# Kernel tuning notes

Hardware: AMD Instinct MI355X
Metric: run time of the kernel (lower is better)

## Reference

```python
import jax, jax.numpy as jnp
import numpy as np

G = 8
NEIGHBORS = 9
EPS = 1e-5


def grid_sample_bilinear_border(img, grid):
    # img: [B, C, H, W], grid: [B, Hg, Wg, 2] with (x, y) in [-1, 1]
    # matches torch.nn.functional.grid_sample(mode='bilinear', padding_mode='border', align_corners=False)
    B, C, H, W = img.shape
    gx, gy = grid[..., 0], grid[..., 1]
    ix = jnp.clip(((gx + 1.0) * W - 1.0) * 0.5, 0.0, W - 1.0)
    iy = jnp.clip(((gy + 1.0) * H - 1.0) * 0.5, 0.0, H - 1.0)
    x0 = jnp.floor(ix); y0 = jnp.floor(iy)
    x1 = x0 + 1.0;      y1 = y0 + 1.0
    w00 = (x1 - ix) * (y1 - iy)
    w01 = (ix - x0) * (y1 - iy)
    w10 = (x1 - ix) * (iy - y0)
    w11 = (ix - x0) * (iy - y0)
    x0i = jnp.clip(x0, 0, W - 1).astype(jnp.int32)
    x1i = jnp.clip(x1, 0, W - 1).astype(jnp.int32)
    y0i = jnp.clip(y0, 0, H - 1).astype(jnp.int32)
    y1i = jnp.clip(y1, 0, H - 1).astype(jnp.int32)

    def gather(im, yy, xx):  # im [C,H,W], yy/xx [Hg,Wg] -> [C,Hg,Wg]
        return im[:, yy, xx]

    g = jax.vmap(gather)
    out = (g(img, y0i, x0i) * w00[:, None]
         + g(img, y0i, x1i) * w01[:, None]
         + g(img, y1i, x0i) * w10[:, None]
         + g(img, y1i, x1i) * w11[:, None])
    return out  # [B, C, Hg, Wg]


def pconv(x, w):
    # 1x1x1 conv3d (no bias): x [B,Cin,D,H,W], w [Cout,Cin]
    return jnp.einsum('bcdhw,oc->bodhw', x, w)


def bn_relu(x, gamma, beta):
    # BatchNorm3d (training-mode batch stats, biased variance) + ReLU
    mean = jnp.mean(x, axis=(0, 2, 3, 4), keepdims=True)
    var = jnp.var(x, axis=(0, 2, 3, 4), keepdims=True)
    xn = (x - mean) * jax.lax.rsqrt(var + EPS)
    return jax.nn.relu(xn * gamma.reshape(1, -1, 1, 1, 1) + beta.reshape(1, -1, 1, 1, 1))


def setup_inputs() -> dict:
    key = jax.random.key(0)
    ks = jax.random.split(key, 8)
    B, C, H, W = 2, 64, 256, 320
    ref_feature = jax.random.normal(ks[0], (B, C, H, W), dtype=jnp.float32)
    grid = jax.random.uniform(ks[1], (B, NEIGHBORS * H, W, 2), dtype=jnp.float32,
                              minval=-1.0, maxval=1.0)
    s0 = 1.0 / np.sqrt(G)
    w0 = jax.random.uniform(ks[2], (16, G), jnp.float32, -s0, s0)
    g0 = jnp.ones((16,), jnp.float32); b0 = jnp.zeros((16,), jnp.float32)
    s1 = 1.0 / np.sqrt(16)
    w1 = jax.random.uniform(ks[3], (8, 16), jnp.float32, -s1, s1)
    g1 = jnp.ones((8,), jnp.float32); b1 = jnp.zeros((8,), jnp.float32)
    s2 = 1.0 / np.sqrt(8)
    ws = jax.random.uniform(ks[4], (1, 8), jnp.float32, -s2, s2)
    bs = jax.random.uniform(ks[5], (1,), jnp.float32, -s2, s2)
    return {"ref_feature": ref_feature, "grid": grid,
            "w0": w0, "g0": g0, "b0": b0,
            "w1": w1, "g1": g1, "b1": b1,
            "ws": ws, "bs": bs}


def reference(ref_feature, grid, w0, g0, b0, w1, g1, b1, ws, bs):
    B, C, H, W = ref_feature.shape
    x = grid_sample_bilinear_border(ref_feature, grid)          # [B, C, 9H, W]
    ref = ref_feature.reshape(B, G, C // G, H, W)               # [B, G, C/G, H, W]
    x = x.reshape(B, G, C // G, NEIGHBORS, H, W)
    x = jnp.mean(x * ref[:, :, :, None], axis=2)                # [B, G, 9, H, W]
    x = bn_relu(pconv(x, w0), g0, b0)                           # [B, 16, 9, H, W]
    x = bn_relu(pconv(x, w1), g1, b1)                           # [B, 8, 9, H, W]
    s = pconv(x, ws) + bs.reshape(1, -1, 1, 1, 1)               # [B, 1, 9, H, W]
    return jax.nn.sigmoid(jnp.squeeze(s, axis=1))               # [B, 9, H, W]
```

## Files before the change

### kernel.cpp

```cpp
#include <hip/hip_runtime.h>
#include <math.h>


constexpr int   Bc  = 2;
constexpr int   Cc  = 64;
constexpr int   Hc  = 256;
constexpr int   Wc  = 320;
constexpr int   NBc = 9;
constexpr int   HWc = Hc * Wc;
constexpr int   NPIX = Bc * HWc;
constexpr int   NPT  = Bc * NBc * HWc;
constexpr float EPSV = 1e-5f;

constexpr int NBLK_S = NPIX / 32;
constexpr int NBT4   = NPT / 1024;

constexpr size_t OFF_FEATB = 0;
constexpr size_t OFF_SB    = OFF_FEATB + (size_t)NPIX * 32;
constexpr size_t OFF_P1    = 0;
constexpr size_t OFF_P2    = OFF_P1 + (size_t)NBT4 * 64;
constexpr size_t OFF_PAR1  = OFF_P2 + (size_t)NBT4 * 16;
constexpr size_t OFF_PAR2  = OFF_PAR1 + 272;

__device__ __forceinline__ unsigned short f2bf_rne(float v) {
  unsigned int u = __float_as_uint(v);
  unsigned int r = (u + 0x7fffu + ((u >> 16) & 1u)) >> 16;
  return (unsigned short)r;
}
__device__ __forceinline__ void unpack8(uint4 u, float f[8]) {
  f[0] = __uint_as_float(u.x << 16);
  f[1] = __uint_as_float(u.x & 0xffff0000u);
  f[2] = __uint_as_float(u.y << 16);
  f[3] = __uint_as_float(u.y & 0xffff0000u);
  f[4] = __uint_as_float(u.z << 16);
  f[5] = __uint_as_float(u.z & 0xffff0000u);
  f[6] = __uint_as_float(u.w << 16);
  f[7] = __uint_as_float(u.w & 0xffff0000u);
}
__device__ __forceinline__ float dot8(const float s[8], float4 wa, float4 wb) {
  return s[0] * wa.x + s[1] * wa.y + s[2] * wa.z + s[3] * wa.w +
         s[4] * wb.x + s[5] * wb.y + s[6] * wb.z + s[7] * wb.w;
}

__global__ __launch_bounds__(256) void k_transpose(
    const float* __restrict__ feat, unsigned short* __restrict__ featB) {
  __shared__ float lds[64][65];
  const int tid  = threadIdx.x;
  const int b    = blockIdx.x / (HWc / 64);
  const int tile = blockIdx.x % (HWc / 64);
  const int hw0  = tile * 64;
  const int p    = tid & 63;
  const int ty   = tid >> 6;

  const float* src = feat + (size_t)b * Cc * HWc + hw0 + p;
#pragma unroll
  for (int c0 = 0; c0 < 64; c0 += 4) {
    lds[c0 + ty][p] = src[(size_t)(c0 + ty) * HWc];
  }
  __syncthreads();
  const int ch = tid & 63;
  unsigned short* dst = featB + ((size_t)b * HWc + hw0) * 64 + ch;
#pragma unroll
  for (int p0 = 0; p0 < 64; p0 += 4) {
    dst[(size_t)(p0 + ty) * 64] = f2bf_rne(lds[ch][p0 + ty]);
  }
}

__global__ __launch_bounds__(256) void k_sample(
    const float* __restrict__ grid, const unsigned short* __restrict__ featB,
    unsigned short* __restrict__ sOut) {
  const int tid = threadIdx.x;
  const int cid = blockIdx.x * 32 + (tid >> 3);
  const int j   = tid & 7;
  const int b   = cid / HWc;
  const int hw  = cid - b * HWc;
  const int h   = hw / Wc;
  const int w   = hw - h * Wc;

  const uint4* fbAll = (const uint4*)featB;
  const uint4 ur = fbAll[(size_t)cid * 8 + j];
  float r[8];
  unpack8(ur, r);

  const uint4* fb = fbAll + (size_t)b * HWc * 8;

#pragma unroll 3
  for (int n = 0; n < NBc; ++n) {
    const size_t gi = ((((size_t)b * NBc + n) * Hc + h) * Wc + w) * 2;
    const float2 g2 = *(const float2*)(grid + gi);
    float ix = ((g2.x + 1.f) * (float)Wc - 1.f) * 0.5f;
    float iy = ((g2.y + 1.f) * (float)Hc - 1.f) * 0.5f;
    ix = fminf(fmaxf(ix, 0.f), (float)(Wc - 1));
    iy = fminf(fmaxf(iy, 0.f), (float)(Hc - 1));
    const float x0f = floorf(ix), y0f = floorf(iy);
    const float fx = ix - x0f, fy = iy - y0f;
    const int x0 = (int)x0f, y0 = (int)y0f;
    const int x1 = min(x0 + 1, Wc - 1), y1 = min(y0 + 1, Hc - 1);
    const float w00 = (1.f - fx) * (1.f - fy);
    const float w01 = fx * (1.f - fy);
    const float w10 = (1.f - fx) * fy;
    const float w11 = fx * fy;

    const uint4 u00 = fb[(size_t)(y0 * Wc + x0) * 8 + j];
    const uint4 u01 = fb[(size_t)(y0 * Wc + x1) * 8 + j];
    const uint4 u10 = fb[(size_t)(y1 * Wc + x0) * 8 + j];
    const uint4 u11 = fb[(size_t)(y1 * Wc + x1) * 8 + j];
    float a[8], c[8], d[8], e[8];
    unpack8(u00, a);
    unpack8(u01, c);
    unpack8(u10, d);
    unpack8(u11, e);

    float s = 0.f;
#pragma unroll
    for (int k = 0; k < 8; ++k) {
      s += (w00 * a[k] + w01 * c[k] + w10 * d[k] + w11 * e[k]) * r[k];
    }
    s *= 0.125f;

    const size_t pt = ((size_t)b * NBc + n) * HWc + hw;
    sOut[pt * 8 + j] = f2bf_rne(s);
  }
}

__global__ __launch_bounds__(256) void k_stats1(
    const unsigned short* __restrict__ sB, float* __restrict__ part1) {
  const int tid = threadIdx.x;
  float acc[44];
#pragma unroll
  for (int i = 0; i < 44; ++i) acc[i] = 0.f;

  const uint4* src = (const uint4*)sB + (size_t)blockIdx.x * 1024 + tid;
#pragma unroll
  for (int i = 0; i < 4; ++i) {
    float s[8];
    unpack8(src[i * 256], s);
#pragma unroll
    for (int j = 0; j < 8; ++j) acc[j] += s[j];
#pragma unroll
    for (int j = 0; j < 8; ++j) {
#pragma unroll
      for (int k = 0; k <= j; ++k) {
        acc[8 + j * (j + 1) / 2 + k] += s[j] * s[k];
      }
    }
  }
  __shared__ float red[4 * 44];
  const int wid = tid >> 6;
#pragma unroll
  for (int i = 0; i < 44; ++i) {
    float v = acc[i];
#pragma unroll
    for (int off = 32; off; off >>= 1) v += __shfl_xor(v, off);
    if ((tid & 63) == 0) red[wid * 44 + i] = v;
  }
  __syncthreads();
  if (tid < 44) {
    part1[blockIdx.x * 64 + tid] =
        red[tid] + red[44 + tid] + red[88 + tid] + red[132 + tid];
  }
}

__global__ __launch_bounds__(256) void k_reduce1(
    const float* __restrict__ part1, const float* __restrict__ w0,
    const float* __restrict__ w1, const float* __restrict__ g0,
    const float* __restrict__ b0, float* __restrict__ par1) {
  __shared__ float red[1024], totm[64], a1s[16];
  const int tid = threadIdx.x;
  {
    const int cq = tid & 15, chk = tid >> 4;
    float4 a = make_float4(0.f, 0.f, 0.f, 0.f);
    for (int r = chk; r < NBT4; r += 16) {
      const float4 v = *(const float4*)(part1 + r * 64 + cq * 4);
      a.x += v.x; a.y += v.y; a.z += v.z; a.w += v.w;
    }
    red[chk * 64 + cq * 4 + 0] = a.x;
    red[chk * 64 + cq * 4 + 1] = a.y;
    red[chk * 64 + cq * 4 + 2] = a.z;
    red[chk * 64 + cq * 4 + 3] = a.w;
  }
  __syncthreads();
  if (tid < 64) {
    float v = 0.f;
#pragma unroll
    for (int k = 0; k < 16; ++k) v += red[k * 64 + tid];
    totm[tid] = v;
  }
  __syncthreads();
  if (tid < 16) {
    float wr[8];
    float mean = 0.f, ey2 = 0.f;
#pragma unroll
    for (int j = 0; j < 8; ++j) {
      wr[j] = w0[tid * 8 + j];
      mean += wr[j] * totm[j];
    }
#pragma unroll
    for (int j = 0; j < 8; ++j) {
#pragma unroll
      for (int k = 0; k <= j; ++k) {
        const float v = wr[j] * wr[k] * totm[8 + j * (j + 1) / 2 + k];
        ey2 += (k == j) ? v : 2.f * v;
      }
    }
    const float invN = 1.f / (float)NPT;
    mean *= invN;
    ey2 *= invN;
    const float var = ey2 - mean * mean;
    const float a = g0[tid] * rsqrtf(var + EPSV);
    a1s[tid] = a;
    par1[128 + tid] = b0[tid] - mean * a;
  }
  __syncthreads();
  if (tid < 128) {
    par1[tid] = a1s[tid >> 3] * w0[tid];
    par1[144 + (tid & 15) * 8 + (tid >> 4)] = w1[tid];
  }
}

__global__ __launch_bounds__(256) void k_stats2(
    const unsigned short* __restrict__ sB, const float* __restrict__ par1,
    float* __restrict__ part2) {
  __shared__ float w0ps[128], c1vs[16], w1ts[128];
  __shared__ float red[64];
  const int tid = threadIdx.x;
  if (tid < 128) {
    w0ps[tid] = par1[tid];
    w1ts[tid] = par1[144 + tid];
  }
  if (tid >= 128 && tid < 144) c1vs[tid - 128] = par1[tid];
  __syncthreads();

  const uint4* src = (const uint4*)sB + (size_t)blockIdx.x * 1024 + tid;
  float s0[8], s1[8], s2[8], s3[8];
  unpack8(src[0], s0);
  unpack8(src[256], s1);
  unpack8(src[512], s2);
  unpack8(src[768], s3);

  float z0[8], z1[8], z2[8], z3[8];
#pragma unroll
  for (int o = 0; o < 8; ++o) { z0[o] = 0.f; z1[o] = 0.f; z2[o] = 0.f; z3[o] = 0.f; }
#pragma unroll
  for (int c = 0; c < 16; ++c) {
    const float4 wa = *(const float4*)(w0ps + c * 8);
    const float4 wb = *(const float4*)(w0ps + c * 8 + 4);
    const float cc = c1vs[c];
    const float4 ta = *(const float4*)(w1ts + c * 8);
    const float4 tb = *(const float4*)(w1ts + c * 8 + 4);
    const float xa = fmaxf(dot8(s0, wa, wb) + cc, 0.f);
    const float xb = fmaxf(dot8(s1, wa, wb) + cc, 0.f);
    const float xc = fmaxf(dot8(s2, wa, wb) + cc, 0.f);
    const float xd = fmaxf(dot8(s3, wa, wb) + cc, 0.f);
    z0[0] += ta.x * xa; z0[1] += ta.y * xa; z0[2] += ta.z * xa; z0[3] += ta.w * xa;
    z0[4] += tb.x * xa; z0[5] += tb.y * xa; z0[6] += tb.z * xa; z0[7] += tb.w * xa;
    z1[0] += ta.x * xb; z1[1] += ta.y * xb; z1[2] += ta.z * xb; z1[3] += ta.w * xb;
    z1[4] += tb.x * xb; z1[5] += tb.y * xb; z1[6] += tb.z * xb; z1[7] += tb.w * xb;
    z2[0] += ta.x * xc; z2[1] += ta.y * xc; z2[2] += ta.z * xc; z2[3] += ta.w * xc;
    z2[4] += tb.x * xc; z2[5] += tb.y * xc; z2[6] += tb.z * xc; z2[7] += tb.w * xc;
    z3[0] += ta.x * xd; z3[1] += ta.y * xd; z3[2] += ta.z * xd; z3[3] += ta.w * xd;
    z3[4] += tb.x * xd; z3[5] += tb.y * xd; z3[6] += tb.z * xd; z3[7] += tb.w * xd;
  }

  const int wid = tid >> 6;
#pragma unroll
  for (int o = 0; o < 8; ++o) {
    float v = (z0[o] + z1[o]) + (z2[o] + z3[o]);
    float v2 = (z0[o] * z0[o] + z1[o] * z1[o]) + (z2[o] * z2[o] + z3[o] * z3[o]);
#pragma unroll
    for (int off = 32; off; off >>= 1) {
      v += __shfl_xor(v, off);
      v2 += __shfl_xor(v2, off);
    }
    if ((tid & 63) == 0) {
      red[wid * 16 + o] = v;
      red[wid * 16 + 8 + o] = v2;
    }
  }
  __syncthreads();
  if (tid < 16) {
    part2[blockIdx.x * 16 + tid] =
        red[tid] + red[16 + tid] + red[32 + tid] + red[48 + tid];
  }
}

__global__ __launch_bounds__(256) void k_reduce2(
    const float* __restrict__ part2, const float* __restrict__ g1,
    const float* __restrict__ b1, const float* __restrict__ wsW,
    const float* __restrict__ bs, float* __restrict__ par2) {
  __shared__ float red[1024], totz[16];
  const int tid = threadIdx.x;
  {
    const int cq = tid & 3, chk = tid >> 2;
    float4 a = make_float4(0.f, 0.f, 0.f, 0.f);
    for (int r = chk; r < NBT4; r += 64) {
      const float4 v = *(const float4*)(part2 + r * 16 + cq * 4);
      a.x += v.x; a.y += v.y; a.z += v.z; a.w += v.w;
    }
    red[chk * 16 + cq * 4 + 0] = a.x;
    red[chk * 16 + cq * 4 + 1] = a.y;
    red[chk * 16 + cq * 4 + 2] = a.z;
    red[chk * 16 + cq * 4 + 3] = a.w;
  }
  __syncthreads();
  if (tid < 16) {
    float v = 0.f;
#pragma unroll
    for (int k = 0; k < 64; ++k) v += red[k * 16 + tid];
    totz[tid] = v;
  }
  __syncthreads();
  if (tid < 8) {
    const float invN = 1.f / (float)NPT;
    const float mean = totz[tid] * invN;
    const float var = totz[8 + tid] * invN - mean * mean;
    const float a = g1[tid] * rsqrtf(var + EPSV);
    par2[tid * 4 + 0] = a;
    par2[tid * 4 + 1] = b1[tid] - mean * a;
    par2[tid * 4 + 2] = wsW[tid];
    par2[tid * 4 + 3] = 0.f;
  }
  if (tid == 8) par2[32] = bs[0];
}

__global__ __launch_bounds__(256) void k_final(
    const unsigned short* __restrict__ sB, const float* __restrict__ par1,
    const float* __restrict__ par2, float* __restrict__ out) {
  __shared__ float w0ps[128], c1vs[16], w1ts[128], w2s[33];
  const int tid = threadIdx.x;
  if (tid < 128) {
    w0ps[tid] = par1[tid];
    w1ts[tid] = par1[144 + tid];
  }
  if (tid >= 128 && tid < 144) c1vs[tid - 128] = par1[tid];
  if (tid >= 160 && tid < 193) w2s[tid - 160] = par2[tid - 160];
  __syncthreads();

  const uint4* src = (const uint4*)sB + (size_t)blockIdx.x * 1024 + tid;
  float s0[8], s1[8], s2[8], s3[8];
  unpack8(src[0], s0);
  unpack8(src[256], s1);
  unpack8(src[512], s2);
  unpack8(src[768], s3);

  float z0[8], z1[8], z2[8], z3[8];
#pragma unroll
  for (int o = 0; o < 8; ++o) { z0[o] = 0.f; z1[o] = 0.f; z2[o] = 0.f; z3[o] = 0.f; }
#pragma unroll
  for (int c = 0; c < 16; ++c) {
    const float4 wa = *(const float4*)(w0ps + c * 8);
    const float4 wb = *(const float4*)(w0ps + c * 8 + 4);
    const float cc = c1vs[c];
    const float4 ta = *(const float4*)(w1ts + c * 8);
    const float4 tb = *(const float4*)(w1ts + c * 8 + 4);
    const float xa = fmaxf(dot8(s0, wa, wb) + cc, 0.f);
    const float xb = fmaxf(dot8(s1, wa, wb) + cc, 0.f);
    const float xc = fmaxf(dot8(s2, wa, wb) + cc, 0.f);
    const float xd = fmaxf(dot8(s3, wa, wb) + cc, 0.f);
    z0[0] += ta.x * xa; z0[1] += ta.y * xa; z0[2] += ta.z * xa; z0[3] += ta.w * xa;
    z0[4] += tb.x * xa; z0[5] += tb.y * xa; z0[6] += tb.z * xa; z0[7] += tb.w * xa;
    z1[0] += ta.x * xb; z1[1] += ta.y * xb; z1[2] += ta.z * xb; z1[3] += ta.w * xb;
    z1[4] += tb.x * xb; z1[5] += tb.y * xb; z1[6] += tb.z * xb; z1[7] += tb.w * xb;
    z2[0] += ta.x * xc; z2[1] += ta.y * xc; z2[2] += ta.z * xc; z2[3] += ta.w * xc;
    z2[4] += tb.x * xc; z2[5] += tb.y * xc; z2[6] += tb.z * xc; z2[7] += tb.w * xc;
    z3[0] += ta.x * xd; z3[1] += ta.y * xd; z3[2] += ta.z * xd; z3[3] += ta.w * xd;
    z3[4] += tb.x * xd; z3[5] += tb.y * xd; z3[6] += tb.z * xd; z3[7] += tb.w * xd;
  }

  const float bsr = w2s[32];
  float r0 = bsr, r1 = bsr, r2 = bsr, r3 = bsr;
#pragma unroll
  for (int o = 0; o < 8; ++o) {
    const float4 pr = *(const float4*)(w2s + o * 4);
    r0 += pr.z * fmaxf(fmaf(pr.x, z0[o], pr.y), 0.f);
    r1 += pr.z * fmaxf(fmaf(pr.x, z1[o], pr.y), 0.f);
    r2 += pr.z * fmaxf(fmaf(pr.x, z2[o], pr.y), 0.f);
    r3 += pr.z * fmaxf(fmaf(pr.x, z3[o], pr.y), 0.f);
  }
  float* op = out + (size_t)blockIdx.x * 1024 + tid;
  op[0]   = 1.f / (1.f + __expf(-r0));
  op[256] = 1.f / (1.f + __expf(-r1));
  op[512] = 1.f / (1.f + __expf(-r2));
  op[768] = 1.f / (1.f + __expf(-r3));
}

extern "C" void kernel_launch(void* const* d_in, const int* in_sizes, int n_in,
                              void* d_out, int out_size, void* d_ws,
                              size_t ws_size, hipStream_t stream) {
  const float* feat = (const float*)d_in[0];
  const float* grid = (const float*)d_in[1];
  const float* w0 = (const float*)d_in[2];
  const float* g0 = (const float*)d_in[3];
  const float* b0 = (const float*)d_in[4];
  const float* w1 = (const float*)d_in[5];
  const float* g1 = (const float*)d_in[6];
  const float* b1 = (const float*)d_in[7];
  const float* wsW = (const float*)d_in[8];
  const float* bs = (const float*)d_in[9];
  float* out = (float*)d_out;

  float* wsf = (float*)d_ws;
  unsigned short* featB = (unsigned short*)(wsf + OFF_FEATB);
  unsigned short* sB    = (unsigned short*)(wsf + OFF_SB);
  float* part1 = wsf + OFF_P1;
  float* part2 = wsf + OFF_P2;
  float* par1  = wsf + OFF_PAR1;
  float* par2  = wsf + OFF_PAR2;

  k_transpose<<<Bc * (HWc / 64), 256, 0, stream>>>(feat, featB);
  k_sample<<<NBLK_S, 256, 0, stream>>>(grid, featB, sB);
  k_stats1<<<NBT4, 256, 0, stream>>>(sB, part1);
  k_reduce1<<<1, 256, 0, stream>>>(part1, w0, w1, g0, b0, par1);
  k_stats2<<<NBT4, 256, 0, stream>>>(sB, par1, part2);
  k_reduce2<<<1, 256, 0, stream>>>(part2, g1, b1, wsW, bs, par2);
  k_final<<<NBT4, 256, 0, stream>>>(sB, par1, par2, out);
}
```

Baseline: 268.1 us.

## Fuse first-layer moment statistics into sampling kernel, drop stats1 pass

The sampling kernel now accumulates the per-point group sums and pairwise products (via lane shuffles over the 8 group lanes) and writes per-block partial moments. This removes the separate k_stats1 pass, which re-read the whole bf16 intermediate. The partials go into the output buffer as scratch, and k_reduce1 now reduces 5120 blocks of 72 floats in a single block with long serial loops. That reduction could become latency-bound. Statistics are now taken from the fp32 values rather than the bf16-rounded ones.

```diff
diff --git a/kernel.cpp b/kernel.cpp
--- a/kernel.cpp
+++ b/kernel.cpp
@@ -17,8 +17,7 @@
 
 constexpr size_t OFF_FEATB = 0;
 constexpr size_t OFF_SB    = OFF_FEATB + (size_t)NPIX * 32;
-constexpr size_t OFF_P1    = 0;
-constexpr size_t OFF_P2    = OFF_P1 + (size_t)NBT4 * 64;
+constexpr size_t OFF_P2    = 0;
 constexpr size_t OFF_PAR1  = OFF_P2 + (size_t)NBT4 * 16;
 constexpr size_t OFF_PAR2  = OFF_PAR1 + 272;
 
@@ -68,7 +67,7 @@
 
 __global__ __launch_bounds__(256) void k_sample(
     const float* __restrict__ grid, const unsigned short* __restrict__ featB,
-    unsigned short* __restrict__ sOut) {
+    unsigned short* __restrict__ sOut, float* __restrict__ partM) {
   const int tid = threadIdx.x;
   const int cid = blockIdx.x * 32 + (tid >> 3);
   const int j   = tid & 7;
@@ -83,6 +82,11 @@
   unpack8(ur, r);
 
   const uint4* fb = fbAll + (size_t)b * HWc * 8;
+
+  float macc[8];
+#pragma unroll
+  for (int m = 0; m < 8; ++m) macc[m] = 0.f;
+  float msum = 0.f;
 
 #pragma unroll 3
   for (int n = 0; n < NBc; ++n) {
@@ -120,87 +124,65 @@
 
     const size_t pt = ((size_t)b * NBc + n) * HWc + hw;
     sOut[pt * 8 + j] = f2bf_rne(s);
-  }
-}
-
-__global__ __launch_bounds__(256) void k_stats1(
-    const unsigned short* __restrict__ sB, float* __restrict__ part1) {
-  const int tid = threadIdx.x;
-  float acc[44];
-#pragma unroll
-  for (int i = 0; i < 44; ++i) acc[i] = 0.f;
-
-  const uint4* src = (const uint4*)sB + (size_t)blockIdx.x * 1024 + tid;
-#pragma unroll
-  for (int i = 0; i < 4; ++i) {
-    float s[8];
-    unpack8(src[i * 256], s);
-#pragma unroll
-    for (int j = 0; j < 8; ++j) acc[j] += s[j];
-#pragma unroll
-    for (int j = 0; j < 8; ++j) {
-#pragma unroll
-      for (int k = 0; k <= j; ++k) {
-        acc[8 + j * (j + 1) / 2 + k] += s[j] * s[k];
-      }
-    }
-  }
-  __shared__ float red[4 * 44];
-  const int wid = tid >> 6;
-#pragma unroll
-  for (int i = 0; i < 44; ++i) {
-    float v = acc[i];
-#pragma unroll
-    for (int off = 32; off; off >>= 1) v += __shfl_xor(v, off);
-    if ((tid & 63) == 0) red[wid * 44 + i] = v;
-  }
-  __syncthreads();
-  if (tid < 44) {
-    part1[blockIdx.x * 64 + tid] =
-        red[tid] + red[44 + tid] + red[88 + tid] + red[132 + tid];
+
+    macc[0] += s * s;
+#pragma unroll
+    for (int m = 1; m < 8; ++m) macc[m] += s * __shfl_xor(s, m);
+    msum += s;
+  }
+
+#pragma unroll
+  for (int m = 0; m < 8; ++m) {
+    macc[m] += __shfl_xor(macc[m], 8);
+    macc[m] += __shfl_xor(macc[m], 16);
+    macc[m] += __shfl_xor(macc[m], 32);
+  }
+  msum += __shfl_xor(msum, 8);
+  msum += __shfl_xor(msum, 16);
+  msum += __shfl_xor(msum, 32);
+
+  __shared__ float mred[4][72];
+  const int lane = tid & 63, wid = tid >> 6;
+  if (lane < 8) {
+#pragma unroll
+    for (int m = 0; m < 8; ++m) mred[wid][lane * 9 + m] = macc[m];
+    mred[wid][lane * 9 + 8] = msum;
+  }
+  __syncthreads();
+  if (tid < 72) {
+    partM[(size_t)blockIdx.x * 72 + tid] =
+        mred[0][tid] + mred[1][tid] + mred[2][tid] + mred[3][tid];
   }
 }
 
 __global__ __launch_bounds__(256) void k_reduce1(
-    const float* __restrict__ part1, const float* __restrict__ w0,
+    const float* __restrict__ partM, const float* __restrict__ w0,
     const float* __restrict__ w1, const float* __restrict__ g0,
     const float* __restrict__ b0, float* __restrict__ par1) {
-  __shared__ float red[1024], totm[64], a1s[16];
-  const int tid = threadIdx.x;
-  {
-    const int cq = tid & 15, chk = tid >> 4;
-    float4 a = make_float4(0.f, 0.f, 0.f, 0.f);
-    for (int r = chk; r < NBT4; r += 16) {
-      const float4 v = *(const float4*)(part1 + r * 64 + cq * 4);
-      a.x += v.x; a.y += v.y; a.z += v.z; a.w += v.w;
-    }
-    red[chk * 64 + cq * 4 + 0] = a.x;
-    red[chk * 64 + cq * 4 + 1] = a.y;
-    red[chk * 64 + cq * 4 + 2] = a.z;
-    red[chk * 64 + cq * 4 + 3] = a.w;
-  }
-  __syncthreads();
-  if (tid < 64) {
-    float v = 0.f;
-#pragma unroll
-    for (int k = 0; k < 16; ++k) v += red[k * 64 + tid];
-    totm[tid] = v;
-  }
+  __shared__ float st[216], tot[72], a1s[16];
+  const int tid = threadIdx.x;
+  if (tid < 216) {
+    const int c = tid % 72, chk = tid / 72;
+    float a = 0.f;
+    for (int r = chk; r < NBLK_S; r += 3) a += partM[(size_t)r * 72 + c];
+    st[tid] = a;
+  }
+  __syncthreads();
+  if (tid < 72) tot[tid] = st[tid] + st[72 + tid] + st[144 + tid];
   __syncthreads();
   if (tid < 16) {
     float wr[8];
     float mean = 0.f, ey2 = 0.f;
 #pragma unroll
-    for (int j = 0; j < 8; ++j) {
-      wr[j] = w0[tid * 8 + j];
-      mean += wr[j] * totm[j];
-    }
-#pragma unroll
-    for (int j = 0; j < 8; ++j) {
-#pragma unroll
-      for (int k = 0; k <= j; ++k) {
-        const float v = wr[j] * wr[k] * totm[8 + j * (j + 1) / 2 + k];
-        ey2 += (k == j) ? v : 2.f * v;
+    for (int jj = 0; jj < 8; ++jj) {
+      wr[jj] = w0[tid * 8 + jj];
+      mean += wr[jj] * tot[jj * 9 + 8];
+    }
+#pragma unroll
+    for (int jj = 0; jj < 8; ++jj) {
+#pragma unroll
+      for (int kk = 0; kk < 8; ++kk) {
+        ey2 += wr[jj] * wr[kk] * tot[jj * 9 + (jj ^ kk)];
       }
     }
     const float invN = 1.f / (float)NPT;
@@ -402,15 +384,14 @@
   float* wsf = (float*)d_ws;
   unsigned short* featB = (unsigned short*)(wsf + OFF_FEATB);
   unsigned short* sB    = (unsigned short*)(wsf + OFF_SB);
-  float* part1 = wsf + OFF_P1;
   float* part2 = wsf + OFF_P2;
   float* par1  = wsf + OFF_PAR1;
   float* par2  = wsf + OFF_PAR2;
+  float* partM = out;
 
   k_transpose<<<Bc * (HWc / 64), 256, 0, stream>>>(feat, featB);
-  k_sample<<<NBLK_S, 256, 0, stream>>>(grid, featB, sB);
-  k_stats1<<<NBT4, 256, 0, stream>>>(sB, part1);
-  k_reduce1<<<1, 256, 0, stream>>>(part1, w0, w1, g0, b0, par1);
+  k_sample<<<NBLK_S, 256, 0, stream>>>(grid, featB, sB, partM);
+  k_reduce1<<<1, 256, 0, stream>>>(partM, w0, w1, g0, b0, par1);
   k_stats2<<<NBT4, 256, 0, stream>>>(sB, par1, part2);
   k_reduce2<<<1, 256, 0, stream>>>(part2, g1, b1, wsW, bs, par2);
   k_final<<<NBT4, 256, 0, stream>>>(sB, par1, par2, out);
```

Result: slower. 624.0 us (+132.7%).
